# Kernel optimization log

Hardware: AMD Instinct MI355X
Metric: run time of the kernel (lower is better)

## Reference

```python
import jax, jax.numpy as jnp
import numpy as np

H = 64  # LSTM hidden size

def _lstm_layer(x, Wih, Whh, bih, bhh):
    # x: [B,T,I]; PyTorch gate order (i, f, g, o); zero initial state
    B, T, _ = x.shape
    pre = jnp.einsum('bti,gi->btg', x, Wih) + bih + bhh  # [B,T,4H]
    def step(carry, p):
        h, c = carry
        g = p + h @ Whh.T
        i, f, gg, o = jnp.split(g, 4, axis=-1)
        c = jax.nn.sigmoid(f) * c + jax.nn.sigmoid(i) * jnp.tanh(gg)
        h = jax.nn.sigmoid(o) * jnp.tanh(c)
        return (h, c), h
    h0 = jnp.zeros((B, H), x.dtype)
    c0 = jnp.zeros((B, H), x.dtype)
    _, hs = jax.lax.scan(step, (h0, c0), jnp.swapaxes(pre, 0, 1))
    return jnp.swapaxes(hs, 0, 1)  # [B,T,H]

def _lstm_params(key, in_dim):
    s = 1.0 / np.sqrt(H)
    k1, k2, k3, k4 = jax.random.split(key, 4)
    return (jax.random.uniform(k1, (4 * H, in_dim), jnp.float32, -s, s),
            jax.random.uniform(k2, (4 * H, H), jnp.float32, -s, s),
            jax.random.uniform(k3, (4 * H,), jnp.float32, -s, s),
            jax.random.uniform(k4, (4 * H,), jnp.float32, -s, s))

def setup_inputs() -> dict:
    key = jax.random.key(0)
    ks = jax.random.split(key, 9)
    B, T = 1024, 1024
    x = jax.random.normal(ks[0], (B, T, 3), jnp.float32)
    e1 = _lstm_params(ks[1], 3)
    e2 = _lstm_params(ks[2], H)
    d1 = _lstm_params(ks[3], 5)
    d2 = _lstm_params(ks[4], H)
    s = 1.0 / np.sqrt(H)
    enc_fc_W = jax.random.uniform(ks[5], (5, H), jnp.float32, -s, s)
    enc_fc_b = jax.random.uniform(ks[6], (5,), jnp.float32, -s, s)
    dec_fc_W = jax.random.uniform(ks[7], (3, H), jnp.float32, -s, s)
    dec_fc_b = jax.random.uniform(ks[8], (3,), jnp.float32, -s, s)
    return {
        'x': x,
        'e1_Wih': e1[0], 'e1_Whh': e1[1], 'e1_bih': e1[2], 'e1_bhh': e1[3],
        'e2_Wih': e2[0], 'e2_Whh': e2[1], 'e2_bih': e2[2], 'e2_bhh': e2[3],
        'enc_fc_W': enc_fc_W, 'enc_fc_b': enc_fc_b,
        'd1_Wih': d1[0], 'd1_Whh': d1[1], 'd1_bih': d1[2], 'd1_bhh': d1[3],
        'd2_Wih': d2[0], 'd2_Whh': d2[1], 'd2_bih': d2[2], 'd2_bhh': d2[3],
        'dec_fc_W': dec_fc_W, 'dec_fc_b': dec_fc_b,
    }

def reference(x,
              e1_Wih, e1_Whh, e1_bih, e1_bhh,
              e2_Wih, e2_Whh, e2_bih, e2_bhh,
              enc_fc_W, enc_fc_b,
              d1_Wih, d1_Whh, d1_bih, d1_bhh,
              d2_Wih, d2_Whh, d2_bih, d2_bhh,
              dec_fc_W, dec_fc_b):
    h = _lstm_layer(x, e1_Wih, e1_Whh, e1_bih, e1_bhh)
    h = _lstm_layer(h, e2_Wih, e2_Whh, e2_bih, e2_bhh)
    u = h[:, -1, :] @ enc_fc_W.T + enc_fc_b        # [B,5]
    u = u[:, None, :]                               # [B,1,5]
    d = _lstm_layer(u, d1_Wih, d1_Whh, d1_bih, d1_bhh)
    d = _lstm_layer(d, d2_Wih, d2_Whh, d2_bih, d2_bhh)
    tau = d[:, -1, :] @ dec_fc_W.T + dec_fc_b       # [B,3]
    return (u, tau)
```

## Files before the change

kernel.cpp:

```cpp
#include <hip/hip_runtime.h>
#include <stdint.h>

typedef _Float16 f16x8 __attribute__((ext_vector_type(8)));
typedef float f32x4 __attribute__((ext_vector_type(4)));

__device__ __forceinline__ float sigf(float x) {
    return __builtin_amdgcn_rcpf(1.0f + __expf(-x));
}
__device__ __forceinline__ float tanhf_fast(float x) {
    return 1.0f - 2.0f * __builtin_amdgcn_rcpf(1.0f + __expf(2.0f * x));
}

__global__ __launch_bounds__(512, 1)
void lstm_mfma16(const float* __restrict__ x,
                 const float* __restrict__ W1i, const float* __restrict__ W1h,
                 const float* __restrict__ b1i, const float* __restrict__ b1h,
                 const float* __restrict__ W2i, const float* __restrict__ W2h,
                 const float* __restrict__ b2i, const float* __restrict__ b2h,
                 const float* __restrict__ eW,  const float* __restrict__ eb,
                 const float* __restrict__ D1i, const float* __restrict__ D1bi,
                 const float* __restrict__ D1bh,
                 const float* __restrict__ D2i, const float* __restrict__ D2bi,
                 const float* __restrict__ D2bh,
                 const float* __restrict__ dW,  const float* __restrict__ db,
                 float* __restrict__ out)
{
    __shared__ __align__(16) _Float16 h1b[2][16][104];
    __shared__ __align__(16) _Float16 h2b[2][16][72];
    __shared__ float uW[8][8];
    __shared__ float tlA[8][64];
    __shared__ float tlB[8][64];

    const int tid = threadIdx.x, blk = blockIdx.x;
    const int wid = tid >> 6, lane = tid & 63;
    const int rl = lane & 15, hi = lane >> 4;
    const bool isL1 = (wid < 4);
    const int w = isL1 ? wid : wid - 4;

    {
        uint32_t* z1 = (uint32_t*)&h1b[0][0][0];
        for (int i = tid; i < 1664; i += 512) z1[i] = 0u;
        uint32_t* z2 = (uint32_t*)&h2b[0][0][0];
        for (int i = tid; i < 1152; i += 512) z2[i] = 0u;
    }

    f16x8 afr[4][4];
    #pragma unroll
    for (int g = 0; g < 4; ++g) {
        const int grow = g * 64 + w * 16 + rl;
        if (isL1) {
            #pragma unroll
            for (int s = 0; s < 2; ++s) {
                f16x8 v;
                #pragma unroll
                for (int i = 0; i < 8; ++i)
                    v[i] = (_Float16)W1h[grow * 64 + s * 32 + hi * 8 + i];
                afr[g][s] = v;
            }
            {
                f16x8 v;
                #pragma unroll
                for (int i = 0; i < 8; ++i) {
                    int kk = hi * 8 + i;
                    v[i] = (kk < 3) ? (_Float16)W1i[grow * 3 + kk] : (_Float16)0.0f;
                }
                afr[g][2] = v;
            }
            {
                f16x8 v;
                #pragma unroll
                for (int i = 0; i < 8; ++i) v[i] = (_Float16)0.0f;
                afr[g][3] = v;
            }
        } else {
            #pragma unroll
            for (int s = 0; s < 2; ++s) {
                f16x8 v;
                #pragma unroll
                for (int i = 0; i < 8; ++i)
                    v[i] = (_Float16)W2i[grow * 64 + s * 32 + hi * 8 + i];
                afr[g][s] = v;
            }
            #pragma unroll
            for (int s = 0; s < 2; ++s) {
                f16x8 v;
                #pragma unroll
                for (int i = 0; i < 8; ++i)
                    v[i] = (_Float16)W2h[grow * 64 + s * 32 + hi * 8 + i];
                afr[g][2 + s] = v;
            }
        }
    }

    f32x4 bias[4];
    #pragma unroll
    for (int g = 0; g < 4; ++g) {
        #pragma unroll
        for (int r = 0; r < 4; ++r) {
            int grow = g * 64 + w * 16 + hi * 4 + r;
            bias[g][r] = isL1 ? (b1i[grow] + b1h[grow]) : (b2i[grow] + b2h[grow]);
        }
    }

    float cst[4] = {0.0f, 0.0f, 0.0f, 0.0f};

    __syncthreads();
    if (wid == 0 && lane < 16) {
        const float* xp = x + (size_t)(blk * 16 + lane) * 3072;
        h1b[0][lane][64] = (_Float16)xp[0];
        h1b[0][lane][65] = (_Float16)xp[1];
        h1b[0][lane][66] = (_Float16)xp[2];
    }
    __syncthreads();

    #pragma unroll 1
    for (int t = 0; t <= 1024; ++t) {
        const int p = t & 1;

        float xf0 = 0.f, xf1 = 0.f, xf2 = 0.f;
        const bool doX = (wid == 0) && (lane < 16) && (t + 1 < 1024);
        if (doX) {
            const float* xp = x + (size_t)(blk * 16 + lane) * 3072 + (size_t)(t + 1) * 3;
            xf0 = xp[0]; xf1 = xp[1]; xf2 = xp[2];
        }

        if (isL1 && t < 1024) {
            f32x4 a0 = bias[0], a1 = bias[1], a2 = bias[2], a3 = bias[3];
            #pragma unroll
            for (int s = 0; s < 3; ++s) {
                f16x8 bf = *(const f16x8*)&h1b[p][rl][s * 32 + hi * 8];
                a0 = __builtin_amdgcn_mfma_f32_16x16x32_f16(afr[0][s], bf, a0, 0, 0, 0);
                a1 = __builtin_amdgcn_mfma_f32_16x16x32_f16(afr[1][s], bf, a1, 0, 0, 0);
                a2 = __builtin_amdgcn_mfma_f32_16x16x32_f16(afr[2][s], bf, a2, 0, 0, 0);
                a3 = __builtin_amdgcn_mfma_f32_16x16x32_f16(afr[3][s], bf, a3, 0, 0, 0);
            }
            uint16_t hu[4];
            #pragma unroll
            for (int r = 0; r < 4; ++r) {
                float pi = a0[r], pf = a1[r], pgg = a2[r], po = a3[r];
                cst[r] = sigf(pf) * cst[r] + sigf(pi) * tanhf_fast(pgg);
                float hn = sigf(po) * tanhf_fast(cst[r]);
                hu[r] = __builtin_bit_cast(uint16_t, (_Float16)hn);
            }
            uint2 pk;
            pk.x = (uint32_t)hu[0] | ((uint32_t)hu[1] << 16);
            pk.y = (uint32_t)hu[2] | ((uint32_t)hu[3] << 16);
            *(uint2*)&h1b[p ^ 1][rl][w * 16 + hi * 4] = pk;
        } else if (!isL1 && t >= 1) {
            f32x4 a0 = bias[0], a1 = bias[1], a2 = bias[2], a3 = bias[3];
            #pragma unroll
            for (int s = 0; s < 2; ++s) {
                f16x8 bf = *(const f16x8*)&h1b[p][rl][s * 32 + hi * 8];
                a0 = __builtin_amdgcn_mfma_f32_16x16x32_f16(afr[0][s], bf, a0, 0, 0, 0);
                a1 = __builtin_amdgcn_mfma_f32_16x16x32_f16(afr[1][s], bf, a1, 0, 0, 0);
                a2 = __builtin_amdgcn_mfma_f32_16x16x32_f16(afr[2][s], bf, a2, 0, 0, 0);
                a3 = __builtin_amdgcn_mfma_f32_16x16x32_f16(afr[3][s], bf, a3, 0, 0, 0);
            }
            #pragma unroll
            for (int s = 0; s < 2; ++s) {
                f16x8 bf = *(const f16x8*)&h2b[p][rl][s * 32 + hi * 8];
                a0 = __builtin_amdgcn_mfma_f32_16x16x32_f16(afr[0][2 + s], bf, a0, 0, 0, 0);
                a1 = __builtin_amdgcn_mfma_f32_16x16x32_f16(afr[1][2 + s], bf, a1, 0, 0, 0);
                a2 = __builtin_amdgcn_mfma_f32_16x16x32_f16(afr[2][2 + s], bf, a2, 0, 0, 0);
                a3 = __builtin_amdgcn_mfma_f32_16x16x32_f16(afr[3][2 + s], bf, a3, 0, 0, 0);
            }
            uint16_t hu[4];
            #pragma unroll
            for (int r = 0; r < 4; ++r) {
                float pi = a0[r], pf = a1[r], pgg = a2[r], po = a3[r];
                cst[r] = sigf(pf) * cst[r] + sigf(pi) * tanhf_fast(pgg);
                float hn = sigf(po) * tanhf_fast(cst[r]);
                hu[r] = __builtin_bit_cast(uint16_t, (_Float16)hn);
            }
            uint2 pk;
            pk.x = (uint32_t)hu[0] | ((uint32_t)hu[1] << 16);
            pk.y = (uint32_t)hu[2] | ((uint32_t)hu[3] << 16);
            *(uint2*)&h2b[p ^ 1][rl][w * 16 + hi * 4] = pk;
        }

        if (doX) {
            h1b[p ^ 1][lane][64] = (_Float16)xf0;
            h1b[p ^ 1][lane][65] = (_Float16)xf1;
            h1b[p ^ 1][lane][66] = (_Float16)xf2;
        }
        __syncthreads();
    }

    #pragma unroll 1
    for (int ss = 0; ss < 2; ++ss) {
        const int s = wid * 2 + ss;
        const int S = blk * 16 + s;

        if (lane < 5) {
            float acc = eb[lane];
            for (int k = 0; k < 64; ++k)
                acc += eW[lane * 64 + k] * (float)h2b[1][s][k];
            uW[wid][lane] = acc;
            out[S * 5 + lane] = acc;
        }
        __syncthreads();

        {
            float u0 = uW[wid][0], u1 = uW[wid][1], u2 = uW[wid][2],
                  u3 = uW[wid][3], u4 = uW[wid][4];
            int ri = lane, rg = 128 + lane, ro = 192 + lane;
            float pi = D1bi[ri] + D1bh[ri];
            float pg = D1bi[rg] + D1bh[rg];
            float po = D1bi[ro] + D1bh[ro];
            pi += D1i[ri*5+0]*u0 + D1i[ri*5+1]*u1 + D1i[ri*5+2]*u2 + D1i[ri*5+3]*u3 + D1i[ri*5+4]*u4;
            pg += D1i[rg*5+0]*u0 + D1i[rg*5+1]*u1 + D1i[rg*5+2]*u2 + D1i[rg*5+3]*u3 + D1i[rg*5+4]*u4;
            po += D1i[ro*5+0]*u0 + D1i[ro*5+1]*u1 + D1i[ro*5+2]*u2 + D1i[ro*5+3]*u3 + D1i[ro*5+4]*u4;
            float cd = sigf(pi) * tanhf_fast(pg);
            float hd = sigf(po) * tanhf_fast(cd);
            tlA[wid][lane] = hd;
        }
        __syncthreads();

        {
            int ri = lane, rg = 128 + lane, ro = 192 + lane;
            float pi = D2bi[ri] + D2bh[ri];
            float pg = D2bi[rg] + D2bh[rg];
            float po = D2bi[ro] + D2bh[ro];
            for (int k = 0; k < 64; ++k) {
                float hk = tlA[wid][k];
                pi += D2i[ri * 64 + k] * hk;
                pg += D2i[rg * 64 + k] * hk;
                po += D2i[ro * 64 + k] * hk;
            }
            float cd = sigf(pi) * tanhf_fast(pg);
            float hd = sigf(po) * tanhf_fast(cd);
            tlB[wid][lane] = hd;
        }
        __syncthreads();

        if (lane < 3) {
            float acc = db[lane];
            for (int k = 0; k < 64; ++k) acc += dW[lane * 64 + k] * tlB[wid][k];
            out[5120 + S * 3 + lane] = acc;
        }
        __syncthreads();
    }
}

extern "C" void kernel_launch(void* const* d_in, const int* in_sizes, int n_in,
                              void* d_out, int out_size, void* d_ws, size_t ws_size,
                              hipStream_t stream) {
    (void)in_sizes; (void)n_in; (void)out_size; (void)d_ws; (void)ws_size;
    const float* x    = (const float*)d_in[0];
    const float* W1i  = (const float*)d_in[1];
    const float* W1h  = (const float*)d_in[2];
    const float* b1i  = (const float*)d_in[3];
    const float* b1h  = (const float*)d_in[4];
    const float* W2i  = (const float*)d_in[5];
    const float* W2h  = (const float*)d_in[6];
    const float* b2i  = (const float*)d_in[7];
    const float* b2h  = (const float*)d_in[8];
    const float* eW   = (const float*)d_in[9];
    const float* eb   = (const float*)d_in[10];
    const float* D1i  = (const float*)d_in[11];
    const float* D1bi = (const float*)d_in[13];
    const float* D1bh = (const float*)d_in[14];
    const float* D2i  = (const float*)d_in[15];
    const float* D2bi = (const float*)d_in[17];
    const float* D2bh = (const float*)d_in[18];
    const float* dW   = (const float*)d_in[19];
    const float* db   = (const float*)d_in[20];

    hipLaunchKernelGGL(lstm_mfma16, dim3(64), dim3(512), 0, stream,
                       x, W1i, W1h, b1i, b1h, W2i, W2h, b2i, b2h, eW, eb,
                       D1i, D1bi, D1bh, D2i, D2bi, D2bh, dW, db,
                       (float*)d_out);
}
```

Baseline: 1.007 ms.

## Prefetch x inputs in 16-step chunks into separate LDS buffer

Input x values are now loaded in batches of 16 timesteps by 256 threads into a double-buffered shared array, rather than one global load per timestep by a single wave. The input projection for layer 1 is done as a separate MFMA over this xs buffer, with zero B fragments for hi>0, and the h1 buffer shrinks to 72 columns. The aim is to take per-step global load latency off the serial recurrence's critical path and cut the first layer's K from 96 to 64 plus a small x tile. In exchange it adds extra LDS, chunk-boundary branching, and a third MFMA group that still runs every step.

```diff
diff --git a/kernel.cpp b/kernel.cpp
--- a/kernel.cpp
+++ b/kernel.cpp
@@ -9,6 +9,11 @@
 }
 __device__ __forceinline__ float tanhf_fast(float x) {
     return 1.0f - 2.0f * __builtin_amdgcn_rcpf(1.0f + __expf(2.0f * x));
+}
+__device__ __forceinline__ uint32_t pk2f(float a, float b) {
+    uint16_t ua = __builtin_bit_cast(uint16_t, (_Float16)a);
+    uint16_t ub = __builtin_bit_cast(uint16_t, (_Float16)b);
+    return (uint32_t)ua | ((uint32_t)ub << 16);
 }
 
 __global__ __launch_bounds__(512, 1)
@@ -25,8 +30,9 @@
                  const float* __restrict__ dW,  const float* __restrict__ db,
                  float* __restrict__ out)
 {
-    __shared__ __align__(16) _Float16 h1b[2][16][104];
+    __shared__ __align__(16) _Float16 h1b[2][16][72];
     __shared__ __align__(16) _Float16 h2b[2][16][72];
+    __shared__ __align__(16) _Float16 xs[2][16][16][8];
     __shared__ float uW[8][8];
     __shared__ float tlA[8][64];
     __shared__ float tlB[8][64];
@@ -39,9 +45,11 @@
 
     {
         uint32_t* z1 = (uint32_t*)&h1b[0][0][0];
-        for (int i = tid; i < 1664; i += 512) z1[i] = 0u;
+        for (int i = tid; i < 1152; i += 512) z1[i] = 0u;
         uint32_t* z2 = (uint32_t*)&h2b[0][0][0];
         for (int i = tid; i < 1152; i += 512) z2[i] = 0u;
+        uint32_t* z3 = (uint32_t*)&xs[0][0][0][0];
+        for (int i = tid; i < 2048; i += 512) z3[i] = 0u;
     }
 
     f16x8 afr[4][4];
@@ -104,35 +112,48 @@
 
     float cst[4] = {0.0f, 0.0f, 0.0f, 0.0f};
 
+    const int tt = tid >> 4, sA = tid & 15;
+    const float* xsrc = x + (size_t)(blk * 16 + sA) * 3072;
+    float xr0 = 0.f, xr1 = 0.f, xr2 = 0.f;
+
     __syncthreads();
-    if (wid == 0 && lane < 16) {
-        const float* xp = x + (size_t)(blk * 16 + lane) * 3072;
-        h1b[0][lane][64] = (_Float16)xp[0];
-        h1b[0][lane][65] = (_Float16)xp[1];
-        h1b[0][lane][66] = (_Float16)xp[2];
+
+    if (tid < 256) {
+        const float* xp = xsrc + (size_t)tt * 3;
+        uint2 pk;
+        pk.x = pk2f(xp[0], xp[1]);
+        pk.y = pk2f(xp[2], 0.0f);
+        *(uint2*)&xs[0][tt][sA][0] = pk;
     }
     __syncthreads();
 
     #pragma unroll 1
     for (int t = 0; t <= 1024; ++t) {
         const int p = t & 1;
-
-        float xf0 = 0.f, xf1 = 0.f, xf2 = 0.f;
-        const bool doX = (wid == 0) && (lane < 16) && (t + 1 < 1024);
-        if (doX) {
-            const float* xp = x + (size_t)(blk * 16 + lane) * 3072 + (size_t)(t + 1) * 3;
-            xf0 = xp[0]; xf1 = xp[1]; xf2 = xp[2];
+        const int cb = (t >> 4) & 1;
+
+        if ((t & 15) == 0 && (t + 16) < 1024 && tid < 256) {
+            const float* xp = xsrc + (size_t)(t + 16 + tt) * 3;
+            xr0 = xp[0]; xr1 = xp[1]; xr2 = xp[2];
         }
 
         if (isL1 && t < 1024) {
             f32x4 a0 = bias[0], a1 = bias[1], a2 = bias[2], a3 = bias[3];
             #pragma unroll
-            for (int s = 0; s < 3; ++s) {
+            for (int s = 0; s < 2; ++s) {
                 f16x8 bf = *(const f16x8*)&h1b[p][rl][s * 32 + hi * 8];
                 a0 = __builtin_amdgcn_mfma_f32_16x16x32_f16(afr[0][s], bf, a0, 0, 0, 0);
                 a1 = __builtin_amdgcn_mfma_f32_16x16x32_f16(afr[1][s], bf, a1, 0, 0, 0);
                 a2 = __builtin_amdgcn_mfma_f32_16x16x32_f16(afr[2][s], bf, a2, 0, 0, 0);
                 a3 = __builtin_amdgcn_mfma_f32_16x16x32_f16(afr[3][s], bf, a3, 0, 0, 0);
+            }
+            {
+                f16x8 bf = {};
+                if (hi == 0) bf = *(const f16x8*)&xs[cb][t & 15][rl][0];
+                a0 = __builtin_amdgcn_mfma_f32_16x16x32_f16(afr[0][2], bf, a0, 0, 0, 0);
+                a1 = __builtin_amdgcn_mfma_f32_16x16x32_f16(afr[1][2], bf, a1, 0, 0, 0);
+                a2 = __builtin_amdgcn_mfma_f32_16x16x32_f16(afr[2][2], bf, a2, 0, 0, 0);
+                a3 = __builtin_amdgcn_mfma_f32_16x16x32_f16(afr[3][2], bf, a3, 0, 0, 0);
             }
             uint16_t hu[4];
             #pragma unroll
@@ -178,10 +199,11 @@
             *(uint2*)&h2b[p ^ 1][rl][w * 16 + hi * 4] = pk;
         }
 
-        if (doX) {
-            h1b[p ^ 1][lane][64] = (_Float16)xf0;
-            h1b[p ^ 1][lane][65] = (_Float16)xf1;
-            h1b[p ^ 1][lane][66] = (_Float16)xf2;
+        if ((t & 15) == 15 && (t + 1) < 1024 && tid < 256) {
+            uint2 pk;
+            pk.x = pk2f(xr0, xr1);
+            pk.y = pk2f(xr2, 0.0f);
+            *(uint2*)&xs[cb ^ 1][tt][sA][0] = pk;
         }
         __syncthreads();
     }
```

Result: faster. 984.0 us (-2.3%).

## Halve sequences per block to 8 and double grid to 128 blocks

Applied to the files above, without the earlier changes.

Each block now handles 8 sequences instead of 16, so the grid grows from 64 to 128 workgroups and occupies more compute units on the device. MFMA tiles stay 16 wide, with half the columns unused. Accumulators are staged through a shared preX buffer so each lane applies the gate nonlinearities to 2 values instead of 4. The x input is fed from registers straight into an MFMA operand rather than through the shared h1b buffer. The cost is wasted MFMA throughput, extra LDS round trips on the serial per-step critical path, and twice as many blocks loading weights.

```diff
diff --git a/kernel.cpp b/kernel.cpp
--- a/kernel.cpp
+++ b/kernel.cpp
@@ -12,21 +12,22 @@
 }
 
 __global__ __launch_bounds__(512, 1)
-void lstm_mfma16(const float* __restrict__ x,
-                 const float* __restrict__ W1i, const float* __restrict__ W1h,
-                 const float* __restrict__ b1i, const float* __restrict__ b1h,
-                 const float* __restrict__ W2i, const float* __restrict__ W2h,
-                 const float* __restrict__ b2i, const float* __restrict__ b2h,
-                 const float* __restrict__ eW,  const float* __restrict__ eb,
-                 const float* __restrict__ D1i, const float* __restrict__ D1bi,
-                 const float* __restrict__ D1bh,
-                 const float* __restrict__ D2i, const float* __restrict__ D2bi,
-                 const float* __restrict__ D2bh,
-                 const float* __restrict__ dW,  const float* __restrict__ db,
-                 float* __restrict__ out)
+void lstm_t8(const float* __restrict__ x,
+             const float* __restrict__ W1i, const float* __restrict__ W1h,
+             const float* __restrict__ b1i, const float* __restrict__ b1h,
+             const float* __restrict__ W2i, const float* __restrict__ W2h,
+             const float* __restrict__ b2i, const float* __restrict__ b2h,
+             const float* __restrict__ eW,  const float* __restrict__ eb,
+             const float* __restrict__ D1i, const float* __restrict__ D1bi,
+             const float* __restrict__ D1bh,
+             const float* __restrict__ D2i, const float* __restrict__ D2bi,
+             const float* __restrict__ D2bh,
+             const float* __restrict__ dW,  const float* __restrict__ db,
+             float* __restrict__ out)
 {
-    __shared__ __align__(16) _Float16 h1b[2][16][104];
+    __shared__ __align__(16) _Float16 h1b[2][16][72];
     __shared__ __align__(16) _Float16 h2b[2][16][72];
+    __shared__ __align__(16) float preX[8][4][8][16];
     __shared__ float uW[8][8];
     __shared__ float tlA[8][64];
     __shared__ float tlB[8][64];
@@ -35,11 +36,13 @@
     const int wid = tid >> 6, lane = tid & 63;
     const int rl = lane & 15, hi = lane >> 4;
     const bool isL1 = (wid < 4);
-    const int w = isL1 ? wid : wid - 4;
+    const int w = wid & 3;
+    const int uu = lane & 15;
+    const int cc = lane >> 4;
 
     {
         uint32_t* z1 = (uint32_t*)&h1b[0][0][0];
-        for (int i = tid; i < 1664; i += 512) z1[i] = 0u;
+        for (int i = tid; i < 1152; i += 512) z1[i] = 0u;
         uint32_t* z2 = (uint32_t*)&h2b[0][0][0];
         for (int i = tid; i < 1152; i += 512) z2[i] = 0u;
     }
@@ -66,12 +69,7 @@
                 }
                 afr[g][2] = v;
             }
-            {
-                f16x8 v;
-                #pragma unroll
-                for (int i = 0; i < 8; ++i) v[i] = (_Float16)0.0f;
-                afr[g][3] = v;
-            }
+            afr[g][3] = f16x8{};
         } else {
             #pragma unroll
             for (int s = 0; s < 2; ++s) {
@@ -102,50 +100,63 @@
         }
     }
 
-    float cst[4] = {0.0f, 0.0f, 0.0f, 0.0f};
-
-    __syncthreads();
-    if (wid == 0 && lane < 16) {
-        const float* xp = x + (size_t)(blk * 16 + lane) * 3072;
-        h1b[0][lane][64] = (_Float16)xp[0];
-        h1b[0][lane][65] = (_Float16)xp[1];
-        h1b[0][lane][66] = (_Float16)xp[2];
-    }
+    float cst0 = 0.0f, cst1 = 0.0f;
+
+    const bool xl = isL1 && (hi == 0) && (rl < 8);
+    const float* xsrc = x + (size_t)(blk * 8 + rl) * 3072;
+    float xc0 = 0.f, xc1 = 0.f, xc2 = 0.f;
+    float xn0 = 0.f, xn1 = 0.f, xn2 = 0.f;
+    if (xl) { xc0 = xsrc[0]; xc1 = xsrc[1]; xc2 = xsrc[2]; }
+
     __syncthreads();
 
     #pragma unroll 1
     for (int t = 0; t <= 1024; ++t) {
         const int p = t & 1;
 
-        float xf0 = 0.f, xf1 = 0.f, xf2 = 0.f;
-        const bool doX = (wid == 0) && (lane < 16) && (t + 1 < 1024);
-        if (doX) {
-            const float* xp = x + (size_t)(blk * 16 + lane) * 3072 + (size_t)(t + 1) * 3;
-            xf0 = xp[0]; xf1 = xp[1]; xf2 = xp[2];
+        if (xl && (t + 1) < 1024) {
+            const float* q = xsrc + (size_t)(t + 1) * 3;
+            xn0 = q[0]; xn1 = q[1]; xn2 = q[2];
         }
 
         if (isL1 && t < 1024) {
             f32x4 a0 = bias[0], a1 = bias[1], a2 = bias[2], a3 = bias[3];
             #pragma unroll
-            for (int s = 0; s < 3; ++s) {
+            for (int s = 0; s < 2; ++s) {
                 f16x8 bf = *(const f16x8*)&h1b[p][rl][s * 32 + hi * 8];
                 a0 = __builtin_amdgcn_mfma_f32_16x16x32_f16(afr[0][s], bf, a0, 0, 0, 0);
                 a1 = __builtin_amdgcn_mfma_f32_16x16x32_f16(afr[1][s], bf, a1, 0, 0, 0);
                 a2 = __builtin_amdgcn_mfma_f32_16x16x32_f16(afr[2][s], bf, a2, 0, 0, 0);
                 a3 = __builtin_amdgcn_mfma_f32_16x16x32_f16(afr[3][s], bf, a3, 0, 0, 0);
             }
-            uint16_t hu[4];
-            #pragma unroll
-            for (int r = 0; r < 4; ++r) {
-                float pi = a0[r], pf = a1[r], pgg = a2[r], po = a3[r];
-                cst[r] = sigf(pf) * cst[r] + sigf(pi) * tanhf_fast(pgg);
-                float hn = sigf(po) * tanhf_fast(cst[r]);
-                hu[r] = __builtin_bit_cast(uint16_t, (_Float16)hn);
-            }
-            uint2 pk;
-            pk.x = (uint32_t)hu[0] | ((uint32_t)hu[1] << 16);
-            pk.y = (uint32_t)hu[2] | ((uint32_t)hu[3] << 16);
-            *(uint2*)&h1b[p ^ 1][rl][w * 16 + hi * 4] = pk;
+            {
+                f16x8 bx = {};
+                if (hi == 0) {
+                    bx[0] = (_Float16)xc0; bx[1] = (_Float16)xc1; bx[2] = (_Float16)xc2;
+                }
+                a0 = __builtin_amdgcn_mfma_f32_16x16x32_f16(afr[0][2], bx, a0, 0, 0, 0);
+                a1 = __builtin_amdgcn_mfma_f32_16x16x32_f16(afr[1][2], bx, a1, 0, 0, 0);
+                a2 = __builtin_amdgcn_mfma_f32_16x16x32_f16(afr[2][2], bx, a2, 0, 0, 0);
+                a3 = __builtin_amdgcn_mfma_f32_16x16x32_f16(afr[3][2], bx, a3, 0, 0, 0);
+            }
+            if (rl < 8) {
+                *(f32x4*)&preX[wid][0][rl][hi * 4] = a0;
+                *(f32x4*)&preX[wid][1][rl][hi * 4] = a1;
+                *(f32x4*)&preX[wid][2][rl][hi * 4] = a2;
+                *(f32x4*)&preX[wid][3][rl][hi * 4] = a3;
+            }
+            {
+                float pi = preX[wid][0][cc][uu],     pf = preX[wid][1][cc][uu];
+                float pg = preX[wid][2][cc][uu],     po = preX[wid][3][cc][uu];
+                cst0 = sigf(pf) * cst0 + sigf(pi) * tanhf_fast(pg);
+                h1b[p ^ 1][cc][w * 16 + uu] = (_Float16)(sigf(po) * tanhf_fast(cst0));
+
+                pi = preX[wid][0][cc + 4][uu];  pf = preX[wid][1][cc + 4][uu];
+                pg = preX[wid][2][cc + 4][uu];  po = preX[wid][3][cc + 4][uu];
+                cst1 = sigf(pf) * cst1 + sigf(pi) * tanhf_fast(pg);
+                h1b[p ^ 1][cc + 4][w * 16 + uu] = (_Float16)(sigf(po) * tanhf_fast(cst1));
+            }
+            xc0 = xn0; xc1 = xn1; xc2 = xn2;
         } else if (!isL1 && t >= 1) {
             f32x4 a0 = bias[0], a1 = bias[1], a2 = bias[2], a3 = bias[3];
             #pragma unroll
@@ -164,81 +175,76 @@
                 a2 = __builtin_amdgcn_mfma_f32_16x16x32_f16(afr[2][2 + s], bf, a2, 0, 0, 0);
                 a3 = __builtin_amdgcn_mfma_f32_16x16x32_f16(afr[3][2 + s], bf, a3, 0, 0, 0);
             }
-            uint16_t hu[4];
-            #pragma unroll
-            for (int r = 0; r < 4; ++r) {
-                float pi = a0[r], pf = a1[r], pgg = a2[r], po = a3[r];
-                cst[r] = sigf(pf) * cst[r] + sigf(pi) * tanhf_fast(pgg);
-                float hn = sigf(po) * tanhf_fast(cst[r]);
-                hu[r] = __builtin_bit_cast(uint16_t, (_Float16)hn);
-            }
-            uint2 pk;
-            pk.x = (uint32_t)hu[0] | ((uint32_t)hu[1] << 16);
-            pk.y = (uint32_t)hu[2] | ((uint32_t)hu[3] << 16);
-            *(uint2*)&h2b[p ^ 1][rl][w * 16 + hi * 4] = pk;
-        }
-
-        if (doX) {
-            h1b[p ^ 1][lane][64] = (_Float16)xf0;
-            h1b[p ^ 1][lane][65] = (_Float16)xf1;
-            h1b[p ^ 1][lane][66] = (_Float16)xf2;
+            if (rl < 8) {
+                *(f32x4*)&preX[wid][0][rl][hi * 4] = a0;
+                *(f32x4*)&preX[wid][1][rl][hi * 4] = a1;
+                *(f32x4*)&preX[wid][2][rl][hi * 4] = a2;
+                *(f32x4*)&preX[wid][3][rl][hi * 4] = a3;
+            }
+            {
+                float pi = preX[wid][0][cc][uu],     pf = preX[wid][1][cc][uu];
+                float pg = preX[wid][2][cc][uu],     po = preX[wid][3][cc][uu];
+                cst0 = sigf(pf) * cst0 + sigf(pi) * tanhf_fast(pg);
+                h2b[p ^ 1][cc][w * 16 + uu] = (_Float16)(sigf(po) * tanhf_fast(cst0));
+
+                pi = preX[wid][0][cc + 4][uu];  pf = preX[wid][1][cc + 4][uu];
+                pg = preX[wid][2][cc + 4][uu];  po = preX[wid][3][cc + 4][uu];
+                cst1 = sigf(pf) * cst1 + sigf(pi) * tanhf_fast(pg);
+                h2b[p ^ 1][cc + 4][w * 16 + uu] = (_Float16)(sigf(po) * tanhf_fast(cst1));
+            }
         }
         __syncthreads();
     }
 
-    #pragma unroll 1
-    for (int ss = 0; ss < 2; ++ss) {
-        const int s = wid * 2 + ss;
-        const int S = blk * 16 + s;
-
-        if (lane < 5) {
-            float acc = eb[lane];
-            for (int k = 0; k < 64; ++k)
-                acc += eW[lane * 64 + k] * (float)h2b[1][s][k];
-            uW[wid][lane] = acc;
-            out[S * 5 + lane] = acc;
-        }
-        __syncthreads();
-
-        {
-            float u0 = uW[wid][0], u1 = uW[wid][1], u2 = uW[wid][2],
-                  u3 = uW[wid][3], u4 = uW[wid][4];
-            int ri = lane, rg = 128 + lane, ro = 192 + lane;
-            float pi = D1bi[ri] + D1bh[ri];
-            float pg = D1bi[rg] + D1bh[rg];
-            float po = D1bi[ro] + D1bh[ro];
-            pi += D1i[ri*5+0]*u0 + D1i[ri*5+1]*u1 + D1i[ri*5+2]*u2 + D1i[ri*5+3]*u3 + D1i[ri*5+4]*u4;
-            pg += D1i[rg*5+0]*u0 + D1i[rg*5+1]*u1 + D1i[rg*5+2]*u2 + D1i[rg*5+3]*u3 + D1i[rg*5+4]*u4;
-            po += D1i[ro*5+0]*u0 + D1i[ro*5+1]*u1 + D1i[ro*5+2]*u2 + D1i[ro*5+3]*u3 + D1i[ro*5+4]*u4;
-            float cd = sigf(pi) * tanhf_fast(pg);
-            float hd = sigf(po) * tanhf_fast(cd);
-            tlA[wid][lane] = hd;
-        }
-        __syncthreads();
-
-        {
-            int ri = lane, rg = 128 + lane, ro = 192 + lane;
-            float pi = D2bi[ri] + D2bh[ri];
-            float pg = D2bi[rg] + D2bh[rg];
-            float po = D2bi[ro] + D2bh[ro];
-            for (int k = 0; k < 64; ++k) {
-                float hk = tlA[wid][k];
-                pi += D2i[ri * 64 + k] * hk;
-                pg += D2i[rg * 64 + k] * hk;
-                po += D2i[ro * 64 + k] * hk;
-            }
-            float cd = sigf(pi) * tanhf_fast(pg);
-            float hd = sigf(po) * tanhf_fast(cd);
-            tlB[wid][lane] = hd;
-        }
-        __syncthreads();
-
-        if (lane < 3) {
-            float acc = db[lane];
-            for (int k = 0; k < 64; ++k) acc += dW[lane * 64 + k] * tlB[wid][k];
-            out[5120 + S * 3 + lane] = acc;
-        }
-        __syncthreads();
+    const int s = wid;
+    const int S = blk * 8 + s;
+
+    if (lane < 5) {
+        float acc = eb[lane];
+        for (int k = 0; k < 64; ++k)
+            acc += eW[lane * 64 + k] * (float)h2b[1][s][k];
+        uW[wid][lane] = acc;
+        out[S * 5 + lane] = acc;
+    }
+    __syncthreads();
+
+    {
+        float u0 = uW[wid][0], u1 = uW[wid][1], u2 = uW[wid][2],
+              u3 = uW[wid][3], u4 = uW[wid][4];
+        int ri = lane, rg = 128 + lane, ro = 192 + lane;
+        float pi = D1bi[ri] + D1bh[ri];
+        float pg = D1bi[rg] + D1bh[rg];
+        float po = D1bi[ro] + D1bh[ro];
+        pi += D1i[ri*5+0]*u0 + D1i[ri*5+1]*u1 + D1i[ri*5+2]*u2 + D1i[ri*5+3]*u3 + D1i[ri*5+4]*u4;
+        pg += D1i[rg*5+0]*u0 + D1i[rg*5+1]*u1 + D1i[rg*5+2]*u2 + D1i[rg*5+3]*u3 + D1i[rg*5+4]*u4;
+        po += D1i[ro*5+0]*u0 + D1i[ro*5+1]*u1 + D1i[ro*5+2]*u2 + D1i[ro*5+3]*u3 + D1i[ro*5+4]*u4;
+        float cd = sigf(pi) * tanhf_fast(pg);
+        float hd = sigf(po) * tanhf_fast(cd);
+        tlA[wid][lane] = hd;
+    }
+    __syncthreads();
+
+    {
+        int ri = lane, rg = 128 + lane, ro = 192 + lane;
+        float pi = D2bi[ri] + D2bh[ri];
+        float pg = D2bi[rg] + D2bh[rg];
+        float po = D2bi[ro] + D2bh[ro];
+        for (int k = 0; k < 64; ++k) {
+            float hk = tlA[wid][k];
+            pi += D2i[ri * 64 + k] * hk;
+            pg += D2i[rg * 64 + k] * hk;
+            po += D2i[ro * 64 + k] * hk;
+        }
+        float cd = sigf(pi) * tanhf_fast(pg);
+        float hd = sigf(po) * tanhf_fast(cd);
+        tlB[wid][lane] = hd;
+    }
+    __syncthreads();
+
+    if (lane < 3) {
+        float acc = db[lane];
+        for (int k = 0; k < 64; ++k) acc += dW[lane * 64 + k] * tlB[wid][k];
+        out[5120 + S * 3 + lane] = acc;
     }
 }
 
@@ -266,7 +272,7 @@
     const float* dW   = (const float*)d_in[19];
     const float* db   = (const float*)d_in[20];
 
-    hipLaunchKernelGGL(lstm_mfma16, dim3(64), dim3(512), 0, stream,
+    hipLaunchKernelGGL(lstm_t8, dim3(128), dim3(512), 0, stream,
                        x, W1i, W1h, b1i, b1h, W2i, W2h, b2i, b2h, eW, eb,
                        D1i, D1bi, D1bh, D2i, D2bi, D2bh, dW, db,
                        (float*)d_out);
```

New measurement: 0.9999 ms. About the same (-0.7%).
